# Optimization experiments

Hardware: AMD Instinct MI355X
Metric: run time of the kernel (lower is better)

Reference implementation:

```python
import jax, jax.numpy as jnp
import numpy as np

EPS_LN = 1e-5
EPS_NORM = 1e-12


def _layernorm(h, g, b):
    mu = jnp.mean(h, axis=-1, keepdims=True)
    var = jnp.mean((h - mu) ** 2, axis=-1, keepdims=True)
    return (h - mu) * jax.lax.rsqrt(var + EPS_LN) * g + b


def _l2norm(h):
    n = jnp.linalg.norm(h, axis=-1, keepdims=True)
    return h / jnp.maximum(n, EPS_NORM)


def setup_inputs() -> dict:
    key = jax.random.key(0)
    ks = jax.random.split(key, 6)
    B, S, D = 8, 4096, 1024
    A, C, dc = 16, 8, 64      # n_anchors, n_comp, d_comp
    apc = A // C              # anchors per compartment = 2
    x = jax.random.normal(ks[0], (B, S, D), jnp.float32)
    anchors = jax.random.normal(ks[1], (A, D), jnp.float32)  # normalized inside forward
    ln_g = jnp.ones((D,), jnp.float32)
    ln_b = jnp.zeros((D,), jnp.float32)
    W1 = jax.random.normal(ks[2], (C, apc, 2 * dc), jnp.float32) / np.sqrt(apc)
    b1 = jnp.zeros((C, 2 * dc), jnp.float32)
    W2 = jax.random.normal(ks[3], (C, 2 * dc, dc), jnp.float32) / np.sqrt(2 * dc)
    b2 = jnp.zeros((C, dc), jnp.float32)
    cg = jnp.ones((C, dc), jnp.float32)
    cb = jnp.zeros((C, dc), jnp.float32)
    Wp = jax.random.normal(ks[4], (C * dc, D), jnp.float32) / np.sqrt(C * dc)
    bp = jnp.zeros((D,), jnp.float32)
    gate = jnp.full((D,), -3.0, jnp.float32)  # gate_init = -3.0
    return dict(x=x, anchors=anchors, ln_g=ln_g, ln_b=ln_b, W1=W1, b1=b1,
                W2=W2, b2=b2, cg=cg, cb=cb, Wp=Wp, bp=bp, gate=gate)


def reference(x, anchors, ln_g, ln_b, W1, b1, W2, b2, cg, cb, Wp, bp, gate):
    B, S, D = x.shape
    C, apc, _ = W1.shape
    dc = W2.shape[-1]
    # LayerNorm then L2-normalize each token
    h = _l2norm(_layernorm(x.reshape(B * S, D), ln_g, ln_b))  # (N, D)
    a = _l2norm(anchors)                                      # (A, D)
    tri = 1.0 - h @ a.T                                       # (N, A)
    # asgn = arange(A) % C -> comp k reads columns [k, k+C, ...]
    g = tri.reshape(-1, apc, C)                               # g[:, j, k] = tri[:, j*C + k]
    u = jnp.einsum('nak,kae->nke', g, W1) + b1                # (N, C, 2*dc)
    u = jnp.square(jnp.maximum(u, 0.0))                       # squared ReLU
    y = jnp.einsum('nke,ked->nkd', u, W2) + b2                # (N, C, dc)
    y = _layernorm(y, cg, cb)                                 # per-comp LayerNorm over dc
    y = y.reshape(-1, C * dc)                                 # concat comps in order
    update = (y @ Wp + bp).reshape(B, S, D)
    return x + jax.nn.sigmoid(gate) * update
```

## Files before the change

kernel.cpp:

```cpp
#include <hip/hip_runtime.h>
#include <hip/hip_bf16.h>

#define DIM 1024
#define NANCH 16
#define NCOMP 8
#define DC 64
#define DC2 128
#define EPS_LN 1e-5f
#define EPS_NORM 1e-12f

typedef __bf16 bf16x8 __attribute__((ext_vector_type(8)));
typedef float f32x4 __attribute__((ext_vector_type(4)));

__global__ __launch_bounds__(256) void knorm_anchors(
    const float* __restrict__ anchors, float* __restrict__ An) {
  int a = blockIdx.x, t = threadIdx.x;
  int lane = t & 63, wid = t >> 6;
  __shared__ float red[4];
  float v[4]; float ss = 0.f;
#pragma unroll
  for (int i = 0; i < 4; i++) {
    v[i] = anchors[a * DIM + t + 256 * i];
    ss += v[i] * v[i];
  }
  for (int off = 32; off; off >>= 1) ss += __shfl_down(ss, off);
  if (lane == 0) red[wid] = ss;
  __syncthreads();
  float inv = 1.f / fmaxf(sqrtf(red[0] + red[1] + red[2] + red[3]), EPS_NORM);
#pragma unroll
  for (int i = 0; i < 4; i++) An[a * DIM + t + 256 * i] = v[i] * inv;
}

__global__ __launch_bounds__(256) void ktrans(
    const float* __restrict__ Wp, __hip_bfloat16* __restrict__ WpT) {
  __shared__ float tile[64][65];
  int bj = blockIdx.x, bk = blockIdx.y;
  int tx = threadIdx.x & 63, ty = threadIdx.x >> 6;
#pragma unroll
  for (int i = 0; i < 16; i++) {
    int r = ty + 4 * i;
    tile[r][tx] = Wp[(size_t)(bk * 64 + r) * DIM + bj * 64 + tx];
  }
  __syncthreads();
#pragma unroll
  for (int i = 0; i < 16; i++) {
    int r = ty + 4 * i;
    WpT[(size_t)(bj * 64 + r) * 512 + bk * 64 + tx] = __float2bfloat16(tile[tx][r]);
  }
}

__global__ __launch_bounds__(256) void kprep(
    const float* __restrict__ W2, const float* __restrict__ An,
    __hip_bfloat16* __restrict__ W2B, __hip_bfloat16* __restrict__ AnB) {
  int id = blockIdx.x * 256 + threadIdx.x;
  if (id < 65536) {
    int j = id & 7, lane = (id >> 3) & 63, ks = (id >> 9) & 3,
        nt = (id >> 11) & 3, k = id >> 13;
    int e = ks * 32 + (lane >> 4) * 8 + j;
    int n = nt * 16 + (lane & 15);
    W2B[id] = __float2bfloat16(W2[k * (DC2 * DC) + e * DC + n]);
  } else {
    int id2 = id - 65536;
    int j = id2 & 7, lane = (id2 >> 3) & 63, ks = id2 >> 9;
    int e = ks * 32 + (lane >> 4) * 8 + j;
    int a = lane & 15;
    AnB[id2] = __float2bfloat16(An[a * DIM + e]);
  }
}

#define LDA_H 1032
__global__ __launch_bounds__(256) void ktoken(
    const float* __restrict__ x, const __hip_bfloat16* __restrict__ AnB,
    const float* __restrict__ ln_g, const float* __restrict__ ln_b,
    const float* __restrict__ W1, const float* __restrict__ b1,
    const __hip_bfloat16* __restrict__ W2B, const float* __restrict__ b2,
    const float* __restrict__ cg, const float* __restrict__ cb,
    __hip_bfloat16* __restrict__ yout) {
  int t = threadIdx.x;
  int lane = t & 63, w = t >> 6;
  int l15 = lane & 15, quad = lane >> 4;
  int n0 = blockIdx.x * 16;

  __shared__ __hip_bfloat16 hu[16 * LDA_H];
  __shared__ float tri_s[16 * 16];
  __shared__ float part[4 * 64 * 4];

  float gv[16], bv[16];
#pragma unroll
  for (int i = 0; i < 16; i++) { gv[i] = ln_g[i * 64 + lane]; bv[i] = ln_b[i * 64 + lane]; }
#pragma unroll
  for (int it = 0; it < 4; it++) {
    int tok = w * 4 + it;
    const float* xr = x + (size_t)(n0 + tok) * DIM;
    float xv[16], s = 0.f, s2 = 0.f;
#pragma unroll
    for (int i = 0; i < 16; i++) {
      float v = xr[i * 64 + lane];
      xv[i] = v; s += v; s2 += v * v;
    }
#pragma unroll
    for (int off = 32; off; off >>= 1) { s += __shfl_xor(s, off); s2 += __shfl_xor(s2, off); }
    float mu = s * (1.f / DIM);
    float rstd = rsqrtf(s2 * (1.f / DIM) - mu * mu + EPS_LN);
    float ss = 0.f;
#pragma unroll
    for (int i = 0; i < 16; i++) {
      float h = (xv[i] - mu) * rstd * gv[i] + bv[i];
      xv[i] = h; ss += h * h;
    }
#pragma unroll
    for (int off = 32; off; off >>= 1) ss += __shfl_xor(ss, off);
    float inv = 1.f / fmaxf(sqrtf(ss), EPS_NORM);
#pragma unroll
    for (int i = 0; i < 16; i++)
      hu[tok * LDA_H + i * 64 + lane] = __float2bfloat16(xv[i] * inv);
  }
  __syncthreads();

  {
    f32x4 tacc = {0.f, 0.f, 0.f, 0.f};
#pragma unroll
    for (int ks = w * 8; ks < w * 8 + 8; ks++) {
      bf16x8 afr = *(const bf16x8*)(&hu[l15 * LDA_H + ks * 32 + quad * 8]);
      bf16x8 bfr = *(const bf16x8*)(&AnB[ks * 512 + lane * 8]);
      tacc = __builtin_amdgcn_mfma_f32_16x16x32_bf16(afr, bfr, tacc, 0, 0, 0);
    }
    *(f32x4*)(&part[(w * 64 + lane) * 4]) = tacc;
  }
  __syncthreads();
  {
    int ln = t & 63, rg = t >> 6;
    float v = part[(0 * 64 + ln) * 4 + rg] + part[(1 * 64 + ln) * 4 + rg] +
              part[(2 * 64 + ln) * 4 + rg] + part[(3 * 64 + ln) * 4 + rg];
    int m = (ln >> 4) * 4 + rg, a = ln & 15;
    tri_s[m * 16 + a] = 1.f - v;
  }
  __syncthreads();

  {
    float w1a[4], w1b[4], b1v[4];
#pragma unroll
    for (int i = 0; i < 4; i++) {
      int idx = i * 256 + t, k = idx >> 7, e = idx & 127;
      w1a[i] = W1[k * 256 + e];
      w1b[i] = W1[k * 256 + 128 + e];
      b1v[i] = b1[idx];
    }
#pragma unroll
    for (int tok = 0; tok < 16; tok++) {
#pragma unroll
      for (int i = 0; i < 4; i++) {
        int idx = i * 256 + t, k = idx >> 7;
        float uu = tri_s[tok * 16 + k] * w1a[i] +
                   tri_s[tok * 16 + 8 + k] * w1b[i] + b1v[i];
        uu = fmaxf(uu, 0.f);
        hu[tok * LDA_H + idx] = __float2bfloat16(uu * uu);
      }
    }
  }
  __syncthreads();

#pragma unroll
  for (int kc = 0; kc < 2; kc++) {
    int k = w * 2 + kc;
    bf16x8 afr[4];
#pragma unroll
    for (int ks = 0; ks < 4; ks++)
      afr[ks] = *(const bf16x8*)(&hu[l15 * LDA_H + k * 128 + ks * 32 + quad * 8]);
    f32x4 acc[4] = {{0,0,0,0},{0,0,0,0},{0,0,0,0},{0,0,0,0}};
#pragma unroll
    for (int nt = 0; nt < 4; nt++) {
#pragma unroll
      for (int ks = 0; ks < 4; ks++) {
        bf16x8 bfr = *(const bf16x8*)(&W2B[(size_t)(((k * 4 + nt) * 4 + ks)) * 512 + lane * 8]);
        acc[nt] = __builtin_amdgcn_mfma_f32_16x16x32_bf16(afr[ks], bfr, acc[nt], 0, 0, 0);
      }
    }
    float vals[4][4], s1[4] = {0,0,0,0}, s2[4] = {0,0,0,0};
#pragma unroll
    for (int nt = 0; nt < 4; nt++) {
      float b2v = b2[k * 64 + nt * 16 + l15];
#pragma unroll
      for (int r = 0; r < 4; r++) {
        float v = acc[nt][r] + b2v;
        vals[nt][r] = v; s1[r] += v; s2[r] += v * v;
      }
    }
#pragma unroll
    for (int r = 0; r < 4; r++) {
#pragma unroll
      for (int off = 1; off < 16; off <<= 1) {
        s1[r] += __shfl_xor(s1[r], off);
        s2[r] += __shfl_xor(s2[r], off);
      }
    }
#pragma unroll
    for (int r = 0; r < 4; r++) {
      float mu = s1[r] * (1.f / DC);
      float rs = rsqrtf(s2[r] * (1.f / DC) - mu * mu + EPS_LN);
      int tokrow = quad * 4 + r;
#pragma unroll
      for (int nt = 0; nt < 4; nt++) {
        int d = nt * 16 + l15;
        float yn = (vals[nt][r] - mu) * rs * cg[k * 64 + d] + cb[k * 64 + d];
        yout[(size_t)(n0 + tokrow) * 512 + k * 64 + d] = __float2bfloat16(yn);
      }
    }
  }
}

#define LDP 72
__global__ __launch_bounds__(256) void kgemm(
    const __hip_bfloat16* __restrict__ Y, const __hip_bfloat16* __restrict__ WpT,
    const float* __restrict__ x, const float* __restrict__ bp,
    const float* __restrict__ gate, float* __restrict__ out) {
  __shared__ alignas(16) __hip_bfloat16 As[128 * LDP];
  __shared__ alignas(16) __hip_bfloat16 Bs[128 * LDP];
  int t = threadIdx.x, lane = t & 63, wid = t >> 6;
  int bm = blockIdx.x, bj = blockIdx.y;
  int wm = (wid >> 1) * 64, wj = (wid & 1) * 64;
  int l15 = lane & 15, quad = lane >> 4;

  f32x4 acc[4][4] = {};

  for (int k0 = 0; k0 < 512; k0 += 64) {
#pragma unroll
    for (int it = 0; it < 4; it++) {
      int c = it * 256 + t;
      int row = c >> 3, col = (c & 7) * 8;
      *(uint4*)(&As[row * LDP + col]) =
          *(const uint4*)(&Y[(size_t)(bm * 128 + row) * 512 + k0 + col]);
      *(uint4*)(&Bs[row * LDP + col]) =
          *(const uint4*)(&WpT[(size_t)(bj * 128 + row) * 512 + k0 + col]);
    }
    __syncthreads();
#pragma unroll
    for (int kk = 0; kk < 64; kk += 32) {
      bf16x8 af[4], bfr[4];
#pragma unroll
      for (int i = 0; i < 4; i++) {
        af[i]  = *(const bf16x8*)(&As[(wm + i * 16 + l15) * LDP + kk + quad * 8]);
        bfr[i] = *(const bf16x8*)(&Bs[(wj + i * 16 + l15) * LDP + kk + quad * 8]);
      }
#pragma unroll
      for (int i = 0; i < 4; i++)
#pragma unroll
        for (int j = 0; j < 4; j++)
          acc[i][j] = __builtin_amdgcn_mfma_f32_16x16x32_bf16(af[i], bfr[j], acc[i][j], 0, 0, 0);
    }
    __syncthreads();
  }

  float sg[4], bpv[4];
#pragma unroll
  for (int j = 0; j < 4; j++) {
    int gc = bj * 128 + wj + j * 16 + l15;
    sg[j] = 1.f / (1.f + expf(-gate[gc]));
    bpv[j] = bp[gc];
  }
#pragma unroll
  for (int i = 0; i < 4; i++) {
#pragma unroll
    for (int j = 0; j < 4; j++) {
      int gc = bj * 128 + wj + j * 16 + l15;
#pragma unroll
      for (int r = 0; r < 4; r++) {
        int gr = bm * 128 + wm + i * 16 + quad * 4 + r;
        size_t idx = (size_t)gr * DIM + gc;
        out[idx] = x[idx] + sg[j] * (acc[i][j][r] + bpv[j]);
      }
    }
  }
}

extern "C" void kernel_launch(void* const* d_in, const int* in_sizes, int n_in,
                              void* d_out, int out_size, void* d_ws, size_t ws_size,
                              hipStream_t stream) {
  const float* x       = (const float*)d_in[0];
  const float* anchors = (const float*)d_in[1];
  const float* ln_g    = (const float*)d_in[2];
  const float* ln_b    = (const float*)d_in[3];
  const float* W1      = (const float*)d_in[4];
  const float* b1      = (const float*)d_in[5];
  const float* W2      = (const float*)d_in[6];
  const float* b2      = (const float*)d_in[7];
  const float* cg      = (const float*)d_in[8];
  const float* cb      = (const float*)d_in[9];
  const float* Wp      = (const float*)d_in[10];
  const float* bp      = (const float*)d_in[11];
  const float* gate    = (const float*)d_in[12];

  int N = in_sizes[0] / DIM;

  char* w = (char*)d_ws;
  size_t off = 0;
  float* An           = (float*)(w + off);           off += 64 << 10;
  __hip_bfloat16* WpT = (__hip_bfloat16*)(w + off);  off += 1 << 20;
  __hip_bfloat16* W2B = (__hip_bfloat16*)(w + off);  off += 128 << 10;
  __hip_bfloat16* AnB = (__hip_bfloat16*)(w + off);  off += 32 << 10;
  __hip_bfloat16* Yb  = (__hip_bfloat16*)(w + off);

  knorm_anchors<<<NANCH, 256, 0, stream>>>(anchors, An);
  ktrans<<<dim3(16, 8), 256, 0, stream>>>(Wp, WpT);
  kprep<<<320, 256, 0, stream>>>(W2, An, W2B, AnB);
  ktoken<<<N / 16, 256, 0, stream>>>(x, AnB, ln_g, ln_b, W1, b1, W2B, b2, cg, cb, Yb);
  kgemm<<<dim3(N / 128, DIM / 128), 256, 0, stream>>>(Yb, WpT, x, bp, gate,
                                                      (float*)d_out);
}
```

Baseline: 358.1 us.

## Pre-swizzle GEMM operands into MFMA fragment layout and load via global_load_lds

Writes Y and Wp in bf16 directly in the 16x32 MFMA fragment order, so the final GEMM can copy whole fragments into LDS with global_load_lds and read them back contiguously, with no padded row tiles. The three prep kernels (anchor norm, Wp transpose, W2/anchor conversion) are merged into one launch. The token kernel now uses float4 loads for x and the LayerNorm parameters and packs its bf16 stores. The aim is to cut launch overhead, LDS bank conflicts and register staging in the GEMM. The catch is that the Wp prep now runs on only 64 blocks with strided scalar reads, and the Y stores become scattered.

After: 366.7 us. 2.4% more time.

```diff
diff --git a/kernel.cpp b/kernel.cpp
--- a/kernel.cpp
+++ b/kernel.cpp
@@ -10,61 +10,59 @@
 #define EPS_NORM 1e-12f
 
 typedef __bf16 bf16x8 __attribute__((ext_vector_type(8)));
+typedef __bf16 bf16x4 __attribute__((ext_vector_type(4)));
 typedef float f32x4 __attribute__((ext_vector_type(4)));
 
-__global__ __launch_bounds__(256) void knorm_anchors(
-    const float* __restrict__ anchors, float* __restrict__ An) {
-  int a = blockIdx.x, t = threadIdx.x;
-  int lane = t & 63, wid = t >> 6;
-  __shared__ float red[4];
-  float v[4]; float ss = 0.f;
-#pragma unroll
-  for (int i = 0; i < 4; i++) {
-    v[i] = anchors[a * DIM + t + 256 * i];
-    ss += v[i] * v[i];
-  }
-  for (int off = 32; off; off >>= 1) ss += __shfl_down(ss, off);
-  if (lane == 0) red[wid] = ss;
-  __syncthreads();
-  float inv = 1.f / fmaxf(sqrtf(red[0] + red[1] + red[2] + red[3]), EPS_NORM);
-#pragma unroll
-  for (int i = 0; i < 4; i++) An[a * DIM + t + 256 * i] = v[i] * inv;
-}
-
-__global__ __launch_bounds__(256) void ktrans(
-    const float* __restrict__ Wp, __hip_bfloat16* __restrict__ WpT) {
-  __shared__ float tile[64][65];
-  int bj = blockIdx.x, bk = blockIdx.y;
-  int tx = threadIdx.x & 63, ty = threadIdx.x >> 6;
-#pragma unroll
-  for (int i = 0; i < 16; i++) {
-    int r = ty + 4 * i;
-    tile[r][tx] = Wp[(size_t)(bk * 64 + r) * DIM + bj * 64 + tx];
-  }
-  __syncthreads();
-#pragma unroll
-  for (int i = 0; i < 16; i++) {
-    int r = ty + 4 * i;
-    WpT[(size_t)(bj * 64 + r) * 512 + bk * 64 + tx] = __float2bfloat16(tile[tx][r]);
-  }
+
+__device__ __forceinline__ void gload16(const void* g, void* l) {
+  __builtin_amdgcn_global_load_lds(
+      (const __attribute__((address_space(1))) unsigned int*)g,
+      (__attribute__((address_space(3))) unsigned int*)l, 16, 0, 0);
 }
 
 __global__ __launch_bounds__(256) void kprep(
-    const float* __restrict__ W2, const float* __restrict__ An,
-    __hip_bfloat16* __restrict__ W2B, __hip_bfloat16* __restrict__ AnB) {
-  int id = blockIdx.x * 256 + threadIdx.x;
-  if (id < 65536) {
+    const float* __restrict__ Wp, const float* __restrict__ anchors,
+    const float* __restrict__ W2,
+    __hip_bfloat16* __restrict__ WpB, __hip_bfloat16* __restrict__ AnB,
+    __hip_bfloat16* __restrict__ W2B) {
+  int b = blockIdx.x, t = threadIdx.x;
+  if (b < 64) {
+    int jt = b, l15 = t & 15, ks = t >> 4;
+    int n = jt * 16 + l15;
+    size_t obase = (size_t)(jt * 16 + ks) * 512 + l15 * 8;
+#pragma unroll
+    for (int rr = 0; rr < 32; rr++) {
+      int k = ks * 32 + rr;
+      WpB[obase + ((rr >> 3) << 7) + (rr & 7)] =
+          __float2bfloat16(Wp[(size_t)k * DIM + n]);
+    }
+  } else if (b == 64) {
+    __shared__ float invn[16];
+    int a = t >> 4, sub = t & 15;
+    float ss = 0.f;
+#pragma unroll 8
+    for (int i = 0; i < 64; i++) {
+      float v = anchors[a * DIM + sub * 64 + i];
+      ss += v * v;
+    }
+#pragma unroll
+    for (int off = 1; off < 16; off <<= 1) ss += __shfl_xor(ss, off);
+    if (sub == 0) invn[a] = 1.f / fmaxf(sqrtf(ss), EPS_NORM);
+    __syncthreads();
+    for (int q = 0; q < 64; q++) {
+      int o = t * 64 + q;
+      int j = o & 7, lane = (o >> 3) & 63, ks = o >> 9;
+      int e = ks * 32 + (lane >> 4) * 8 + j;
+      int aa = lane & 15;
+      AnB[o] = __float2bfloat16(anchors[aa * DIM + e] * invn[aa]);
+    }
+  } else {
+    int id = (b - 65) * 256 + t;
     int j = id & 7, lane = (id >> 3) & 63, ks = (id >> 9) & 3,
         nt = (id >> 11) & 3, k = id >> 13;
     int e = ks * 32 + (lane >> 4) * 8 + j;
     int n = nt * 16 + (lane & 15);
     W2B[id] = __float2bfloat16(W2[k * (DC2 * DC) + e * DC + n]);
-  } else {
-    int id2 = id - 65536;
-    int j = id2 & 7, lane = (id2 >> 3) & 63, ks = id2 >> 9;
-    int e = ks * 32 + (lane >> 4) * 8 + j;
-    int a = lane & 15;
-    AnB[id2] = __float2bfloat16(An[a * DIM + e]);
   }
 }
 
@@ -75,7 +73,7 @@
     const float* __restrict__ W1, const float* __restrict__ b1,
     const __hip_bfloat16* __restrict__ W2B, const float* __restrict__ b2,
     const float* __restrict__ cg, const float* __restrict__ cb,
-    __hip_bfloat16* __restrict__ yout) {
+    __hip_bfloat16* __restrict__ Ys) {
   int t = threadIdx.x;
   int lane = t & 63, w = t >> 6;
   int l15 = lane & 15, quad = lane >> 4;
@@ -85,18 +83,24 @@
   __shared__ float tri_s[16 * 16];
   __shared__ float part[4 * 64 * 4];
 
-  float gv[16], bv[16];
-#pragma unroll
-  for (int i = 0; i < 16; i++) { gv[i] = ln_g[i * 64 + lane]; bv[i] = ln_b[i * 64 + lane]; }
+  float4 gvv[4], bvv[4];
+#pragma unroll
+  for (int i = 0; i < 4; i++) {
+    gvv[i] = ((const float4*)ln_g)[i * 64 + lane];
+    bvv[i] = ((const float4*)ln_b)[i * 64 + lane];
+  }
 #pragma unroll
   for (int it = 0; it < 4; it++) {
     int tok = w * 4 + it;
-    const float* xr = x + (size_t)(n0 + tok) * DIM;
-    float xv[16], s = 0.f, s2 = 0.f;
-#pragma unroll
-    for (int i = 0; i < 16; i++) {
-      float v = xr[i * 64 + lane];
-      xv[i] = v; s += v; s2 += v * v;
+    const float4* xr4 = (const float4*)(x + (size_t)(n0 + tok) * DIM);
+    float4 xv[4];
+    float s = 0.f, s2 = 0.f;
+#pragma unroll
+    for (int i = 0; i < 4; i++) {
+      float4 v = xr4[i * 64 + lane];
+      xv[i] = v;
+      s += v.x + v.y + v.z + v.w;
+      s2 += v.x * v.x + v.y * v.y + v.z * v.z + v.w * v.w;
     }
 #pragma unroll
     for (int off = 32; off; off >>= 1) { s += __shfl_xor(s, off); s2 += __shfl_xor(s2, off); }
@@ -104,16 +108,23 @@
     float rstd = rsqrtf(s2 * (1.f / DIM) - mu * mu + EPS_LN);
     float ss = 0.f;
 #pragma unroll
-    for (int i = 0; i < 16; i++) {
-      float h = (xv[i] - mu) * rstd * gv[i] + bv[i];
-      xv[i] = h; ss += h * h;
+    for (int i = 0; i < 4; i++) {
+      float4 g = gvv[i], bb = bvv[i], v = xv[i];
+      v.x = (v.x - mu) * rstd * g.x + bb.x; v.y = (v.y - mu) * rstd * g.y + bb.y;
+      v.z = (v.z - mu) * rstd * g.z + bb.z; v.w = (v.w - mu) * rstd * g.w + bb.w;
+      xv[i] = v;
+      ss += v.x * v.x + v.y * v.y + v.z * v.z + v.w * v.w;
     }
 #pragma unroll
     for (int off = 32; off; off >>= 1) ss += __shfl_xor(ss, off);
     float inv = 1.f / fmaxf(sqrtf(ss), EPS_NORM);
 #pragma unroll
-    for (int i = 0; i < 16; i++)
-      hu[tok * LDA_H + i * 64 + lane] = __float2bfloat16(xv[i] * inv);
+    for (int i = 0; i < 4; i++) {
+      bf16x4 hb;
+      hb[0] = (__bf16)(xv[i].x * inv); hb[1] = (__bf16)(xv[i].y * inv);
+      hb[2] = (__bf16)(xv[i].z * inv); hb[3] = (__bf16)(xv[i].w * inv);
+      *(bf16x4*)(&hu[tok * LDA_H + i * 256 + lane * 4]) = hb;
+    }
   }
   __syncthreads();
 
@@ -198,49 +209,51 @@
     for (int r = 0; r < 4; r++) {
       float mu = s1[r] * (1.f / DC);
       float rs = rsqrtf(s2[r] * (1.f / DC) - mu * mu + EPS_LN);
-      int tokrow = quad * 4 + r;
+      int m = quad * 4 + r;
 #pragma unroll
       for (int nt = 0; nt < 4; nt++) {
         int d = nt * 16 + l15;
         float yn = (vals[nt][r] - mu) * rs * cg[k * 64 + d] + cb[k * 64 + d];
-        yout[(size_t)(n0 + tokrow) * 512 + k * 64 + d] = __float2bfloat16(yn);
-      }
-    }
-  }
-}
-
-#define LDP 72
+        int kk = k * 64 + d;
+        int ks = kk >> 5, km = kk & 31;
+        Ys[(size_t)(blockIdx.x * 16 + ks) * 512 + m * 8 + ((km >> 3) << 7) + (km & 7)]
+            = __float2bfloat16(yn);
+      }
+    }
+  }
+}
+
 __global__ __launch_bounds__(256) void kgemm(
-    const __hip_bfloat16* __restrict__ Y, const __hip_bfloat16* __restrict__ WpT,
+    const __hip_bfloat16* __restrict__ Ys, const __hip_bfloat16* __restrict__ WpB,
     const float* __restrict__ x, const float* __restrict__ bp,
     const float* __restrict__ gate, float* __restrict__ out) {
-  __shared__ alignas(16) __hip_bfloat16 As[128 * LDP];
-  __shared__ alignas(16) __hip_bfloat16 Bs[128 * LDP];
+  __shared__ alignas(16) __hip_bfloat16 As[16 * 512];
+  __shared__ alignas(16) __hip_bfloat16 Bs[16 * 512];
   int t = threadIdx.x, lane = t & 63, wid = t >> 6;
   int bm = blockIdx.x, bj = blockIdx.y;
-  int wm = (wid >> 1) * 64, wj = (wid & 1) * 64;
   int l15 = lane & 15, quad = lane >> 4;
 
   f32x4 acc[4][4] = {};
 
   for (int k0 = 0; k0 < 512; k0 += 64) {
+    int ks0 = k0 >> 5;
 #pragma unroll
     for (int it = 0; it < 4; it++) {
-      int c = it * 256 + t;
-      int row = c >> 3, col = (c & 7) * 8;
-      *(uint4*)(&As[row * LDP + col]) =
-          *(const uint4*)(&Y[(size_t)(bm * 128 + row) * 512 + k0 + col]);
-      *(uint4*)(&Bs[row * LDP + col]) =
-          *(const uint4*)(&WpT[(size_t)(bj * 128 + row) * 512 + k0 + col]);
+      int c = wid * 4 + it;
+      int tl = c >> 1, s = c & 1;
+      gload16(Ys + ((size_t)(bm * 8 + tl) * 16 + ks0 + s) * 512 + lane * 8,
+              &As[c * 512]);
+      gload16(WpB + ((size_t)(bj * 8 + tl) * 16 + ks0 + s) * 512 + lane * 8,
+              &Bs[c * 512]);
     }
     __syncthreads();
 #pragma unroll
-    for (int kk = 0; kk < 64; kk += 32) {
+    for (int s = 0; s < 2; s++) {
       bf16x8 af[4], bfr[4];
 #pragma unroll
       for (int i = 0; i < 4; i++) {
-        af[i]  = *(const bf16x8*)(&As[(wm + i * 16 + l15) * LDP + kk + quad * 8]);
-        bfr[i] = *(const bf16x8*)(&Bs[(wj + i * 16 + l15) * LDP + kk + quad * 8]);
+        af[i]  = *(const bf16x8*)(&As[((((wid >> 1) * 4 + i) << 1) + s) * 512 + lane * 8]);
+        bfr[i] = *(const bf16x8*)(&Bs[((((wid & 1) * 4 + i) << 1) + s) * 512 + lane * 8]);
       }
 #pragma unroll
       for (int i = 0; i < 4; i++)
@@ -251,6 +264,7 @@
     __syncthreads();
   }
 
+  int wm = (wid >> 1) * 64, wj = (wid & 1) * 64;
   float sg[4], bpv[4];
 #pragma unroll
   for (int j = 0; j < 4; j++) {
@@ -294,16 +308,13 @@
 
   char* w = (char*)d_ws;
   size_t off = 0;
-  float* An           = (float*)(w + off);           off += 64 << 10;
-  __hip_bfloat16* WpT = (__hip_bfloat16*)(w + off);  off += 1 << 20;
+  __hip_bfloat16* AnB = (__hip_bfloat16*)(w + off);  off += 32 << 10;
+  __hip_bfloat16* WpB = (__hip_bfloat16*)(w + off);  off += 1 << 20;
   __hip_bfloat16* W2B = (__hip_bfloat16*)(w + off);  off += 128 << 10;
-  __hip_bfloat16* AnB = (__hip_bfloat16*)(w + off);  off += 32 << 10;
-  __hip_bfloat16* Yb  = (__hip_bfloat16*)(w + off);
-
-  knorm_anchors<<<NANCH, 256, 0, stream>>>(anchors, An);
-  ktrans<<<dim3(16, 8), 256, 0, stream>>>(Wp, WpT);
-  kprep<<<320, 256, 0, stream>>>(W2, An, W2B, AnB);
-  ktoken<<<N / 16, 256, 0, stream>>>(x, AnB, ln_g, ln_b, W1, b1, W2B, b2, cg, cb, Yb);
-  kgemm<<<dim3(N / 128, DIM / 128), 256, 0, stream>>>(Yb, WpT, x, bp, gate,
+  __hip_bfloat16* Ys  = (__hip_bfloat16*)(w + off);
+
+  kprep<<<321, 256, 0, stream>>>(Wp, anchors, W2, WpB, AnB, W2B);
+  ktoken<<<N / 16, 256, 0, stream>>>(x, AnB, ln_g, ln_b, W1, b1, W2B, b2, cg, cb, Ys);
+  kgemm<<<dim3(N / 128, DIM / 128), 256, 0, stream>>>(Ys, WpB, x, bp, gate,
                                                       (float*)d_out);
 }
```
